# Optimization experiments

Measured on AMD Instinct MI355X. Metric: run time of the kernel, lower is better.

Reference implementation:

```python
import jax, jax.numpy as jnp
import numpy as np

B, I, H, L, D, O = 2048, 512, 512, 32, 1024, 512
TEMP = 1.0


def _make_params(key):
    ks = jax.random.split(key, 16)
    s = 0.05
    p = {}
    p['in_W'] = jax.random.normal(ks[0], (H, I), jnp.float32) * s
    p['in_b'] = jnp.zeros((H,), jnp.float32)
    p['out_W'] = jax.random.normal(ks[1], (O, H), jnp.float32) * s
    p['out_b'] = jnp.zeros((O,), jnp.float32)
    p['enc_Wih'] = jax.random.normal(ks[2], (4 * H, H), jnp.float32) * s
    p['enc_Whh'] = jax.random.normal(ks[3], (4 * H, H), jnp.float32) * s
    p['enc_bih'] = jnp.zeros((4 * H,), jnp.float32)
    p['enc_bhh'] = jnp.zeros((4 * H,), jnp.float32)
    p['dec_Wih'] = jax.random.normal(ks[4], (4 * H, H), jnp.float32) * s
    p['dec_Whh'] = jax.random.normal(ks[5], (4 * H, H), jnp.float32) * s
    p['dec_bih'] = jnp.zeros((4 * H,), jnp.float32)
    p['dec_bhh'] = jnp.zeros((4 * H,), jnp.float32)
    p['h2t_W'] = jax.random.normal(ks[6], (D, H), jnp.float32) * s
    p['h2t_b'] = jnp.zeros((D,), jnp.float32)
    p['t2h_W'] = jax.random.normal(ks[7], (H, D), jnp.float32) * s
    p['t2h_b'] = jnp.zeros((H,), jnp.float32)
    return p


def setup_inputs() -> dict:
    key = jax.random.key(0)
    k1, k2, k3 = jax.random.split(key, 3)
    inp = {'x': jax.random.normal(k1, (B, I), jnp.float32),
           'gumbel': jax.random.gumbel(k2, (L, B, D), jnp.float32)}
    inp.update(_make_params(k3))
    return inp


def _lstm_cell(x, h, c, Wih, Whh, bih, bhh):
    gates = x @ Wih.T + bih + h @ Whh.T + bhh  # [B, 4H]
    i, f, g, o = jnp.split(gates, 4, axis=-1)
    i = jax.nn.sigmoid(i); f = jax.nn.sigmoid(f)
    g = jnp.tanh(g); o = jax.nn.sigmoid(o)
    c_new = f * c + i * g
    h_new = o * jnp.tanh(c_new)
    return h_new, c_new


def reference(x, gumbel, in_W, in_b, out_W, out_b,
              enc_Wih, enc_Whh, enc_bih, enc_bhh,
              dec_Wih, dec_Whh, dec_bih, dec_bhh,
              h2t_W, h2t_b, t2h_W, t2h_b):
    # ---- encode ----
    x_emb = x @ in_W.T + in_b                      # [B, H]
    hx0 = jnp.zeros((B, H), x.dtype)
    inp0 = jnp.zeros((B, H), x.dtype)

    def enc_step(carry, g_noise):
        hx, cx, inp = carry
        hx, cx = _lstm_cell(inp, hx, cx, enc_Wih, enc_Whh, enc_bih, enc_bhh)
        pre = hx @ h2t_W.T + h2t_b                 # [B, D]
        soft = jax.nn.softmax((pre + g_noise) / TEMP, axis=-1)
        amax = jnp.argmax(soft, axis=-1)           # [B]
        oh = jax.nn.one_hot(amax, D, dtype=soft.dtype)
        z = soft + jax.lax.stop_gradient(oh - soft)  # straight-through
        inp = z @ t2h_W.T + t2h_b
        return (hx, cx, inp), (z, pre, amax)

    # initial cell state is the embedded input (cx = x), per the source
    _, (z_seq, logit_seq, msg_seq) = jax.lax.scan(
        enc_step, (hx0, x_emb, inp0), gumbel)
    one_hot = jnp.transpose(z_seq, (1, 0, 2))      # [B, L, D]
    logits = jnp.transpose(logit_seq, (1, 0, 2))   # [B, L, D]
    messages = msg_seq.T                           # [B, L]

    # ---- decode ----
    z_emb = z_seq @ t2h_W.T + t2h_b                # [L, B, H]

    def dec_step(carry, inp):
        hx, cx = carry
        hx, cx = _lstm_cell(inp, hx, cx, dec_Wih, dec_Whh, dec_bih, dec_bhh)
        return (hx, cx), None

    (hx_final, _), _ = jax.lax.scan(
        dec_step, (jnp.zeros((B, H), x.dtype), jnp.zeros((B, H), x.dtype)), z_emb)
    recon = hx_final @ out_W.T + out_b             # [B, O]
    return recon, one_hot, logits, messages
```

## Files before the change

kernel.cpp:

```cpp
#include <hip/hip_runtime.h>
#include <math.h>

#define B_  2048
#define I_  512
#define H_  512
#define L_  32
#define D_  1024
#define O_  512
#define H4_ 2048
#define KC  32

typedef _Float16 f16x8 __attribute__((ext_vector_type(8)));
typedef _Float16 f16x4 __attribute__((ext_vector_type(4)));
typedef float    f32x4 __attribute__((ext_vector_type(4)));

#define SPLIT_S  1024.0f
#define SPLIT_RS 0.0009765625f

__device__ __forceinline__ void gload16(const _Float16* g, _Float16* l) {
    __builtin_amdgcn_global_load_lds(
        (const __attribute__((address_space(1))) void*)g,
        (__attribute__((address_space(3))) void*)l, 16, 0, 0);
}

__device__ __forceinline__ f16x8 lds_frag(const _Float16* base, int row, int ko) {
    int off = row * 64 + ((((ko >> 3) ^ (row & 7))) << 3);
    return *(const f16x8*)(base + off);
}

__global__ __launch_bounds__(256) void gemm_atb(
    const float* __restrict__ A, const float* __restrict__ W,
    const float* __restrict__ bias, float* __restrict__ C, int ldc,
    float* __restrict__ C2, int ldc2,
    int M, int N, int K)
{
    __shared__ __align__(16) float As[KC][68];
    __shared__ __align__(16) float Ws[KC][68];
    const int tx = threadIdx.x & 15, ty = threadIdx.x >> 4;
    const int m0 = blockIdx.y * 64, n0 = blockIdx.x * 64;
    float acc[4][4] = {};

    for (int k0 = 0; k0 < K; k0 += KC) {
#pragma unroll
        for (int p = 0; p < 2; ++p) {
            int q = threadIdx.x + 256 * p;
            int r = q >> 3, c = q & 7;
            float4 va = *reinterpret_cast<const float4*>(
                &A[(long long)(m0 + r) * K + k0 + c * 4]);
            As[c * 4 + 0][r] = va.x; As[c * 4 + 1][r] = va.y;
            As[c * 4 + 2][r] = va.z; As[c * 4 + 3][r] = va.w;
            float4 vw = *reinterpret_cast<const float4*>(
                &W[(long long)(n0 + r) * K + k0 + c * 4]);
            Ws[c * 4 + 0][r] = vw.x; Ws[c * 4 + 1][r] = vw.y;
            Ws[c * 4 + 2][r] = vw.z; Ws[c * 4 + 3][r] = vw.w;
        }
        __syncthreads();
#pragma unroll
        for (int kk = 0; kk < KC; ++kk) {
            float4 a = *reinterpret_cast<const float4*>(&As[kk][ty * 4]);
            float4 w = *reinterpret_cast<const float4*>(&Ws[kk][tx * 4]);
            float av[4] = {a.x, a.y, a.z, a.w};
            float wv[4] = {w.x, w.y, w.z, w.w};
#pragma unroll
            for (int i = 0; i < 4; ++i)
#pragma unroll
                for (int j = 0; j < 4; ++j)
                    acc[i][j] = fmaf(av[i], wv[j], acc[i][j]);
        }
        __syncthreads();
    }

#pragma unroll
    for (int i = 0; i < 4; ++i) {
        int m = m0 + ty * 4 + i;
        int n = n0 + tx * 4;
        float4 out;
        out.x = acc[i][0]; out.y = acc[i][1]; out.z = acc[i][2]; out.w = acc[i][3];
        if (bias) {
            out.x += bias[n + 0]; out.y += bias[n + 1];
            out.z += bias[n + 2]; out.w += bias[n + 3];
        }
        *reinterpret_cast<float4*>(&C[(long long)m * ldc + n]) = out;
        if (C2)
            *reinterpret_cast<float4*>(&C2[(long long)m * ldc2 + n]) = out;
    }
}

__global__ __launch_bounds__(256) void split_f16(
    const float* __restrict__ src, _Float16* __restrict__ d1,
    _Float16* __restrict__ d2, int n4)
{
    int i = blockIdx.x * 256 + threadIdx.x;
    if (i >= n4) return;
    float4 v = reinterpret_cast<const float4*>(src)[i];
    float vv[4] = {v.x, v.y, v.z, v.w};
    f16x4 o1, o2;
#pragma unroll
    for (int j = 0; j < 4; ++j) {
        _Float16 hh = (_Float16)vv[j];
        o1[j] = hh;
        o2[j] = (_Float16)((vv[j] - (float)hh) * SPLIT_S);
    }
    *reinterpret_cast<f16x4*>(d1 + 4 * i) = o1;
    *reinterpret_cast<f16x4*>(d2 + 4 * i) = o2;
}

__global__ __launch_bounds__(256) void gemm_mfma_atb(
    const _Float16* __restrict__ A1, const _Float16* __restrict__ A2,
    const _Float16* __restrict__ W1, const _Float16* __restrict__ W2,
    float* __restrict__ C, int N, int K)
{
    __shared__ __align__(16) _Float16 As1[64 * 64];
    __shared__ __align__(16) _Float16 As2[64 * 64];
    __shared__ __align__(16) _Float16 Ws1[64 * 64];
    __shared__ __align__(16) _Float16 Ws2[64 * 64];

    const int tid = threadIdx.x;
    const int m0 = blockIdx.y * 64, n0 = blockIdx.x * 64;
    const int ln = tid & 63, wid = tid >> 6;
    const int wm = wid >> 1, wn = wid & 1;

    f32x4 accM[2][2] = {};
    f32x4 accC[2][2] = {};

    for (int k0 = 0; k0 < K; k0 += 64) {
        int jsw = ((ln & 7) ^ (ln >> 3)) << 3;
#pragma unroll
        for (int s = 0; s < 2; ++s) {
            int seg = wid + s * 4;
            int r   = seg * 8 + (ln >> 3);
            size_t ga = (size_t)(m0 + r) * K + k0 + jsw;
            gload16(A1 + ga, &As1[seg * 512]);
            gload16(A2 + ga, &As2[seg * 512]);
            size_t gw = (size_t)(n0 + r) * K + k0 + jsw;
            gload16(W1 + gw, &Ws1[seg * 512]);
            gload16(W2 + gw, &Ws2[seg * 512]);
        }
        __syncthreads();
        const int ac = (ln >> 4) << 3;
        const int arow = wm * 32 + (ln & 15);
        const int brow = wn * 32 + (ln & 15);
#pragma unroll
        for (int kc = 0; kc < 2; ++kc) {
            int ko = kc * 32 + ac;
            f16x8 b1[2], b2[2];
#pragma unroll
            for (int fn = 0; fn < 2; ++fn) {
                b1[fn] = lds_frag(Ws1, brow + fn * 16, ko);
                b2[fn] = lds_frag(Ws2, brow + fn * 16, ko);
            }
#pragma unroll
            for (int fm = 0; fm < 2; ++fm) {
                f16x8 a1 = lds_frag(As1, arow + fm * 16, ko);
                f16x8 a2 = lds_frag(As2, arow + fm * 16, ko);
#pragma unroll
                for (int fn = 0; fn < 2; ++fn) {
                    accM[fm][fn] = __builtin_amdgcn_mfma_f32_16x16x32_f16(
                        a1, b1[fn], accM[fm][fn], 0, 0, 0);
                    accC[fm][fn] = __builtin_amdgcn_mfma_f32_16x16x32_f16(
                        a1, b2[fn], accC[fm][fn], 0, 0, 0);
                    accC[fm][fn] = __builtin_amdgcn_mfma_f32_16x16x32_f16(
                        a2, b1[fn], accC[fm][fn], 0, 0, 0);
                }
            }
        }
        __syncthreads();
    }

    const int hl = ln & 15;
    const int rb = m0 + wm * 32 + ((ln >> 4) << 2);
#pragma unroll
    for (int fn = 0; fn < 2; ++fn) {
        int d = n0 + wn * 32 + fn * 16 + hl;
#pragma unroll
        for (int fm = 0; fm < 2; ++fm)
#pragma unroll
            for (int rg = 0; rg < 4; ++rg) {
                int b = rb + fm * 16 + rg;
                C[(size_t)b * N + d] =
                    accM[fm][fn][rg] + SPLIT_RS * accC[fm][fn][rg];
            }
    }
}

__global__ __launch_bounds__(256) void lstm_fused(
    const _Float16* __restrict__ ehx1, const _Float16* __restrict__ ehx2,
    float* __restrict__ ecx,
    const _Float16* __restrict__ eW1, const _Float16* __restrict__ eW2,
    const float* __restrict__ Pe,
    const float* __restrict__ ebih, const float* __restrict__ ebhh,
    _Float16* __restrict__ eho1, _Float16* __restrict__ eho2,
    const _Float16* __restrict__ dhx1, const _Float16* __restrict__ dhx2,
    float* __restrict__ dcx,
    const _Float16* __restrict__ dW1, const _Float16* __restrict__ dW2,
    const float* __restrict__ Pd,
    const float* __restrict__ dbih, const float* __restrict__ dbhh,
    _Float16* __restrict__ dho1, _Float16* __restrict__ dho2,
    float* __restrict__ hof,
    const float* __restrict__ pbest, const int* __restrict__ pidx,
    int have_gather,
    float* __restrict__ onehot, float* __restrict__ messages, int lmsg,
    int encdec)
{
    __shared__ __align__(16) _Float16 As1[64 * 64];
    __shared__ __align__(16) _Float16 As2[64 * 64];
    __shared__ __align__(16) _Float16 Ws1[128 * 64];
    __shared__ __align__(16) _Float16 Ws2[128 * 64];
    __shared__ int ms[64];

    const int tid = threadIdx.x;
    const int m0 = blockIdx.y * 64, h0 = blockIdx.x * 32;
    const int ln = tid & 63, wid = tid >> 6;
    const int wm = wid >> 1, wn = wid & 1;
    const int role = (encdec == 3) ? (int)blockIdx.z : ((encdec & 1) ? 0 : 1);

    const _Float16* hx1 = role ? dhx1 : ehx1;
    const _Float16* hx2 = role ? dhx2 : ehx2;
    float*          cx  = role ? dcx  : ecx;
    const _Float16* W1  = role ? dW1  : eW1;
    const _Float16* W2  = role ? dW2  : eW2;
    const float*    P   = role ? Pd   : Pe;
    const float*    bih = role ? dbih : ebih;
    const float*    bhh = role ? dbhh : ebhh;
    _Float16*       ho1 = role ? dho1 : eho1;
    _Float16*       ho2 = role ? dho2 : eho2;

    if (have_gather && tid < 64) {
        int b = m0 + tid;
        const float* pb = pbest + (size_t)b * 16;
        const int*   pi = pidx  + (size_t)b * 16;
        float best = -INFINITY; int bi = 0;
#pragma unroll
        for (int j = 0; j < 16; ++j) {
            float v = pb[j]; int i = pi[j];
            if (v > best || (v == best && i < bi)) { best = v; bi = i; }
        }
        ms[tid] = bi;
        if (lmsg >= 0 && blockIdx.z == 0 && blockIdx.x == 0) {
            messages[(size_t)b * L_ + lmsg] = (float)bi;
            onehot[((size_t)b * L_ + lmsg) * D_ + bi] = 1.0f;
        }
    }

    f32x4 accM[2][4] = {};
    f32x4 accC[2][4] = {};

    for (int k0 = 0; k0 < H_; k0 += 64) {
        int jsw = ((ln & 7) ^ (ln >> 3)) << 3;
#pragma unroll
        for (int s = 0; s < 2; ++s) {
            int seg = wid + s * 4;
            int r   = seg * 8 + (ln >> 3);
            size_t ga = (size_t)(m0 + r) * H_ + k0 + jsw;
            gload16(hx1 + ga, &As1[seg * 512]);
            gload16(hx2 + ga, &As2[seg * 512]);
        }
#pragma unroll
        for (int s = 0; s < 4; ++s) {
            int seg = wid + s * 4;
            int r   = seg * 8 + (ln >> 3);
            int wrow = ((r >> 4) & 3) * H_ + h0 + ((r >> 6) << 4) + (r & 15);
            size_t gw = (size_t)wrow * H_ + k0 + jsw;
            gload16(W1 + gw, &Ws1[seg * 512]);
            gload16(W2 + gw, &Ws2[seg * 512]);
        }
        __syncthreads();
        const int ac = (ln >> 4) << 3;
        const int arow = wm * 32 + (ln & 15);
        const int brow = wn * 64 + (ln & 15);
#pragma unroll
        for (int kc = 0; kc < 2; ++kc) {
            int ko = kc * 32 + ac;
            f16x8 b1[4], b2[4];
#pragma unroll
            for (int fn = 0; fn < 4; ++fn) {
                b1[fn] = lds_frag(Ws1, brow + fn * 16, ko);
                b2[fn] = lds_frag(Ws2, brow + fn * 16, ko);
            }
#pragma unroll
            for (int fm = 0; fm < 2; ++fm) {
                f16x8 a1 = lds_frag(As1, arow + fm * 16, ko);
                f16x8 a2 = lds_frag(As2, arow + fm * 16, ko);
#pragma unroll
                for (int fn = 0; fn < 4; ++fn) {
                    accM[fm][fn] = __builtin_amdgcn_mfma_f32_16x16x32_f16(
                        a1, b1[fn], accM[fm][fn], 0, 0, 0);
                    accC[fm][fn] = __builtin_amdgcn_mfma_f32_16x16x32_f16(
                        a1, b2[fn], accC[fm][fn], 0, 0, 0);
                    accC[fm][fn] = __builtin_amdgcn_mfma_f32_16x16x32_f16(
                        a2, b1[fn], accC[fm][fn], 0, 0, 0);
                }
            }
        }
        __syncthreads();
    }

    const int hl = ln & 15;
    const int h  = h0 + wn * 16 + hl;
    const int rb = m0 + wm * 32 + ((ln >> 4) << 2);
    float bs0 = bih[0 * H_ + h] + bhh[0 * H_ + h];
    float bs1 = bih[1 * H_ + h] + bhh[1 * H_ + h];
    float bs2 = bih[2 * H_ + h] + bhh[2 * H_ + h];
    float bs3 = bih[3 * H_ + h] + bhh[3 * H_ + h];
#pragma unroll
    for (int fm = 0; fm < 2; ++fm) {
#pragma unroll
        for (int rg = 0; rg < 4; ++rg) {
            int b = rb + fm * 16 + rg;
            float g0 = accM[fm][0][rg] + SPLIT_RS * accC[fm][0][rg] + bs0;
            float g1 = accM[fm][1][rg] + SPLIT_RS * accC[fm][1][rg] + bs1;
            float g2 = accM[fm][2][rg] + SPLIT_RS * accC[fm][2][rg] + bs2;
            float g3 = accM[fm][3][rg] + SPLIT_RS * accC[fm][3][rg] + bs3;
            if (have_gather) {
                const float* Pr = P + (size_t)ms[b - m0] * H4_;
                g0 += Pr[0 * H_ + h]; g1 += Pr[1 * H_ + h];
                g2 += Pr[2 * H_ + h]; g3 += Pr[3 * H_ + h];
            }
            float ig = 1.f / (1.f + expf(-g0));
            float fg = 1.f / (1.f + expf(-g1));
            float gg = tanhf(g2);
            float og = 1.f / (1.f + expf(-g3));
            size_t off = (size_t)b * H_ + h;
            float cnew = fg * cx[off] + ig * gg;
            cx[off] = cnew;
            float hv = og * tanhf(cnew);
            _Float16 hh1 = (_Float16)hv;
            ho1[off] = hh1;
            ho2[off] = (_Float16)((hv - (float)hh1) * SPLIT_S);
            if (role && hof != nullptr) hof[off] = hv;
        }
    }
}

__global__ __launch_bounds__(256) void gemm_pre_fused(
    const _Float16* __restrict__ A1, const _Float16* __restrict__ A2,
    const _Float16* __restrict__ W1, const _Float16* __restrict__ W2,
    const float* __restrict__ bias,
    float* __restrict__ C2, int ldc2,
    const float* __restrict__ gum,
    float* __restrict__ pbest, int* __restrict__ pidx)
{
    __shared__ __align__(16) _Float16 As1[64 * 64];
    __shared__ __align__(16) _Float16 As2[64 * 64];
    __shared__ __align__(16) _Float16 Ws1[64 * 64];
    __shared__ __align__(16) _Float16 Ws2[64 * 64];
    __shared__ float cb[2][64];
    __shared__ int   ci[2][64];

    const int tid = threadIdx.x;
    const int m0 = blockIdx.y * 64, n0 = blockIdx.x * 64;
    const int ln = tid & 63, wid = tid >> 6;
    const int wm = wid >> 1, wn = wid & 1;

    f32x4 accM[2][2] = {};
    f32x4 accC[2][2] = {};

    for (int k0 = 0; k0 < H_; k0 += 64) {
        int jsw = ((ln & 7) ^ (ln >> 3)) << 3;
#pragma unroll
        for (int s = 0; s < 2; ++s) {
            int seg = wid + s * 4;
            int r   = seg * 8 + (ln >> 3);
            size_t ga = (size_t)(m0 + r) * H_ + k0 + jsw;
            gload16(A1 + ga, &As1[seg * 512]);
            gload16(A2 + ga, &As2[seg * 512]);
        }
#pragma unroll
        for (int s = 0; s < 2; ++s) {
            int seg = wid + s * 4;
            int r   = seg * 8 + (ln >> 3);
            size_t gw = (size_t)(n0 + r) * H_ + k0 + jsw;
            gload16(W1 + gw, &Ws1[seg * 512]);
            gload16(W2 + gw, &Ws2[seg * 512]);
        }
        __syncthreads();
        const int ac = (ln >> 4) << 3;
        const int arow = wm * 32 + (ln & 15);
        const int brow = wn * 32 + (ln & 15);
#pragma unroll
        for (int kc = 0; kc < 2; ++kc) {
            int ko = kc * 32 + ac;
            f16x8 b1[2], b2[2];
#pragma unroll
            for (int fn = 0; fn < 2; ++fn) {
                b1[fn] = lds_frag(Ws1, brow + fn * 16, ko);
                b2[fn] = lds_frag(Ws2, brow + fn * 16, ko);
            }
#pragma unroll
            for (int fm = 0; fm < 2; ++fm) {
                f16x8 a1 = lds_frag(As1, arow + fm * 16, ko);
                f16x8 a2 = lds_frag(As2, arow + fm * 16, ko);
#pragma unroll
                for (int fn = 0; fn < 2; ++fn) {
                    accM[fm][fn] = __builtin_amdgcn_mfma_f32_16x16x32_f16(
                        a1, b1[fn], accM[fm][fn], 0, 0, 0);
                    accC[fm][fn] = __builtin_amdgcn_mfma_f32_16x16x32_f16(
                        a1, b2[fn], accC[fm][fn], 0, 0, 0);
                    accC[fm][fn] = __builtin_amdgcn_mfma_f32_16x16x32_f16(
                        a2, b1[fn], accC[fm][fn], 0, 0, 0);
                }
            }
        }
        __syncthreads();
    }

    const int hl = ln & 15;
    const int g4 = ln >> 4;
    const int rb = m0 + wm * 32 + (g4 << 2);
    float vbest[2][4]; int vidx[2][4];
#pragma unroll
    for (int fm = 0; fm < 2; ++fm)
#pragma unroll
        for (int rg = 0; rg < 4; ++rg) { vbest[fm][rg] = -INFINITY; vidx[fm][rg] = 0; }

#pragma unroll
    for (int fn = 0; fn < 2; ++fn) {
        int d = n0 + wn * 32 + fn * 16 + hl;
        float bv = bias[d];
#pragma unroll
        for (int fm = 0; fm < 2; ++fm)
#pragma unroll
            for (int rg = 0; rg < 4; ++rg) {
                int b = rb + fm * 16 + rg;
                float v = accM[fm][fn][rg] + SPLIT_RS * accC[fm][fn][rg] + bv;
                C2[(size_t)b * ldc2 + d] = v;
                float t = v + gum[(size_t)b * D_ + d];
                if (t > vbest[fm][rg]) { vbest[fm][rg] = t; vidx[fm][rg] = d; }
            }
    }

#pragma unroll
    for (int off = 1; off < 16; off <<= 1) {
#pragma unroll
        for (int fm = 0; fm < 2; ++fm)
#pragma unroll
            for (int rg = 0; rg < 4; ++rg) {
                float ov = __shfl_xor(vbest[fm][rg], off);
                int   oi = __shfl_xor(vidx[fm][rg], off);
                if (ov > vbest[fm][rg] ||
                    (ov == vbest[fm][rg] && oi < vidx[fm][rg])) {
                    vbest[fm][rg] = ov; vidx[fm][rg] = oi;
                }
            }
    }
    if (hl == 0) {
#pragma unroll
        for (int fm = 0; fm < 2; ++fm)
#pragma unroll
            for (int rg = 0; rg < 4; ++rg) {
                int rl = wm * 32 + fm * 16 + (g4 << 2) + rg;
                cb[wn][rl] = vbest[fm][rg];
                ci[wn][rl] = vidx[fm][rg];
            }
    }
    __syncthreads();
    if (tid < 64) {
        float b0 = cb[0][tid]; int i0 = ci[0][tid];
        float b1v = cb[1][tid]; int i1 = ci[1][tid];
        if (b1v > b0 || (b1v == b0 && i1 < i0)) { b0 = b1v; i0 = i1; }
        pbest[(size_t)(m0 + tid) * 16 + blockIdx.x] = b0;
        pidx [(size_t)(m0 + tid) * 16 + blockIdx.x] = i0;
    }
}

__global__ __launch_bounds__(256) void build_emb(
    const float* __restrict__ t2h_W, const float* __restrict__ t2h_b,
    float* __restrict__ emb)
{
    int idx = blockIdx.x * 256 + threadIdx.x;
    int d = idx >> 9, h = idx & (H_ - 1);
    emb[idx] = t2h_W[(long long)h * D_ + d] + t2h_b[h];
}

extern "C" void kernel_launch(void* const* d_in, const int* in_sizes, int n_in,
                              void* d_out, int out_size, void* d_ws, size_t ws_size,
                              hipStream_t stream)
{
    (void)in_sizes; (void)n_in; (void)out_size; (void)ws_size;
    const float* x       = (const float*)d_in[0];
    const float* gumbel  = (const float*)d_in[1];
    const float* in_W    = (const float*)d_in[2];
    const float* in_b    = (const float*)d_in[3];
    const float* out_W   = (const float*)d_in[4];
    const float* out_b   = (const float*)d_in[5];
    const float* enc_Wih = (const float*)d_in[6];
    const float* enc_Whh = (const float*)d_in[7];
    const float* enc_bih = (const float*)d_in[8];
    const float* enc_bhh = (const float*)d_in[9];
    const float* dec_Wih = (const float*)d_in[10];
    const float* dec_Whh = (const float*)d_in[11];
    const float* dec_bih = (const float*)d_in[12];
    const float* dec_bhh = (const float*)d_in[13];
    const float* h2t_W   = (const float*)d_in[14];
    const float* h2t_b   = (const float*)d_in[15];
    const float* t2h_W   = (const float*)d_in[16];
    const float* t2h_b   = (const float*)d_in[17];

    float* out      = (float*)d_out;
    float* recon    = out;
    float* onehot   = out + (size_t)B_ * O_;
    float* logits   = onehot + (size_t)B_ * L_ * D_;
    float* messages = logits + (size_t)B_ * L_ * D_;

    float* ws    = (float*)d_ws;
    float* ecx   = ws;
    float* dcx   = ecx + (size_t)B_ * H_;
    float* emb   = dcx + (size_t)B_ * H_;
    float* P_enc = emb + (size_t)D_ * H_;
    float* P_dec = P_enc + (size_t)D_ * H4_;
    float* hxf   = P_dec + (size_t)D_ * H4_;
    float* pbest = hxf + (size_t)B_ * H_;
    int*   pidx  = (int*)(pbest + (size_t)B_ * 16);
    _Float16* fb   = (_Float16*)(pidx + (size_t)B_ * 16);
    _Float16* ehA1 = fb;  fb += (size_t)B_ * H_;
    _Float16* ehA2 = fb;  fb += (size_t)B_ * H_;
    _Float16* ehB1 = fb;  fb += (size_t)B_ * H_;
    _Float16* ehB2 = fb;  fb += (size_t)B_ * H_;
    _Float16* dhA1 = fb;  fb += (size_t)B_ * H_;
    _Float16* dhA2 = fb;  fb += (size_t)B_ * H_;
    _Float16* dhB1 = fb;  fb += (size_t)B_ * H_;
    _Float16* dhB2 = fb;  fb += (size_t)B_ * H_;
    _Float16* encW1 = fb; fb += (size_t)H4_ * H_;
    _Float16* encW2 = fb; fb += (size_t)H4_ * H_;
    _Float16* decW1 = fb; fb += (size_t)H4_ * H_;
    _Float16* decW2 = fb; fb += (size_t)H4_ * H_;
    _Float16* h2t1  = fb; fb += (size_t)D_ * H_;
    _Float16* h2t2  = fb; fb += (size_t)D_ * H_;
    _Float16* embs1 = fb; fb += (size_t)D_ * H_;
    _Float16* embs2 = fb; fb += (size_t)D_ * H_;
    _Float16* eWih1 = fb; fb += (size_t)H4_ * H_;
    _Float16* eWih2 = fb; fb += (size_t)H4_ * H_;
    _Float16* dWih1 = fb; fb += (size_t)H4_ * H_;
    _Float16* dWih2 = fb;

    const dim3 blk256(256);

    (void)hipMemsetAsync(ehA1, 0, (size_t)B_ * H_ * 4, stream);
    (void)hipMemsetAsync(dhA1, 0, (size_t)B_ * H_ * 4, stream);
    (void)hipMemsetAsync(dcx, 0, (size_t)B_ * H_ * sizeof(float), stream);
    (void)hipMemsetAsync(onehot, 0, (size_t)B_ * L_ * D_ * sizeof(float), stream);

    split_f16<<<dim3((H4_ * H_ / 4) / 256), blk256, 0, stream>>>(
        enc_Whh, encW1, encW2, H4_ * H_ / 4);
    split_f16<<<dim3((H4_ * H_ / 4) / 256), blk256, 0, stream>>>(
        dec_Whh, decW1, decW2, H4_ * H_ / 4);
    split_f16<<<dim3((D_ * H_ / 4) / 256), blk256, 0, stream>>>(
        h2t_W, h2t1, h2t2, D_ * H_ / 4);
    split_f16<<<dim3((H4_ * H_ / 4) / 256), blk256, 0, stream>>>(
        enc_Wih, eWih1, eWih2, H4_ * H_ / 4);
    split_f16<<<dim3((H4_ * H_ / 4) / 256), blk256, 0, stream>>>(
        dec_Wih, dWih1, dWih2, H4_ * H_ / 4);

    gemm_atb<<<dim3(H_ / 64, B_ / 64), blk256, 0, stream>>>(
        x, in_W, in_b, ecx, H_, nullptr, 0, B_, H_, I_);

    build_emb<<<dim3((D_ * H_) / 256), blk256, 0, stream>>>(t2h_W, t2h_b, emb);
    split_f16<<<dim3((D_ * H_ / 4) / 256), blk256, 0, stream>>>(
        emb, embs1, embs2, D_ * H_ / 4);
    gemm_mfma_atb<<<dim3(H4_ / 64, D_ / 64), blk256, 0, stream>>>(
        embs1, embs2, eWih1, eWih2, P_enc, H4_, H_);
    gemm_mfma_atb<<<dim3(H4_ / 64, D_ / 64), blk256, 0, stream>>>(
        embs1, embs2, dWih1, dWih2, P_dec, H4_, H_);

    _Float16* e1[2] = {ehA1, ehB1};
    _Float16* e2[2] = {ehA2, ehB2};
    _Float16* d1[2] = {dhA1, dhB1};
    _Float16* d2[2] = {dhA2, dhB2};

    for (int l = 0; l < L_; ++l) {
        int ein = l & 1, eo = ein ^ 1;
        int din = (l - 1) & 1, do_ = din ^ 1;
        lstm_fused<<<dim3(H_ / 32, B_ / 64, l ? 2 : 1), blk256, 0, stream>>>(
            e1[ein], e2[ein], ecx, encW1, encW2, P_enc, enc_bih, enc_bhh,
            e1[eo], e2[eo],
            l ? d1[din] : nullptr, l ? d2[din] : nullptr, dcx,
            decW1, decW2, P_dec, dec_bih, dec_bhh,
            l ? d1[do_] : nullptr, l ? d2[do_] : nullptr,
            nullptr, pbest, pidx, l ? 1 : 0,
            onehot, messages, l - 1, l ? 3 : 1);
        gemm_pre_fused<<<dim3(D_ / 64, B_ / 64), blk256, 0, stream>>>(
            e1[eo], e2[eo], h2t1, h2t2, h2t_b,
            logits + (size_t)l * D_, L_ * D_,
            gumbel + (size_t)l * B_ * D_, pbest, pidx);
    }

    lstm_fused<<<dim3(H_ / 32, B_ / 64, 1), blk256, 0, stream>>>(
        nullptr, nullptr, ecx, encW1, encW2, P_enc, enc_bih, enc_bhh,
        nullptr, nullptr,
        d1[1], d2[1], dcx, decW1, decW2, P_dec, dec_bih, dec_bhh,
        d1[0], d2[0],
        hxf, pbest, pidx, 1,
        onehot, messages, L_ - 1, 2);

    gemm_atb<<<dim3(O_ / 64, B_ / 64), blk256, 0, stream>>>(
        hxf, out_W, out_b, recon, O_, nullptr, 0, B_, O_, H_);
}
```

Before: 2.848 ms.

## Move input/output projections to split-fp16 MFMA and enlarge LSTM row tile

Replaces the scalar fp32 GEMM used for the input embedding and the final output projection with the split-fp16 MFMA GEMM, adding a bias epilogue and split kernels for x, in_W and out_W. The output projection now reads the fp16 hi/lo hidden state directly, so the fp32 final-hidden buffer is dropped. Separately, the fused LSTM kernel now tiles 128 batch rows per block instead of 64, doubling accumulators and LDS use. The aim is more reuse of the recurrent weight tile across rows, at the cost of half as many blocks and higher register and LDS pressure.

```diff
diff --git a/kernel.cpp b/kernel.cpp
--- a/kernel.cpp
+++ b/kernel.cpp
@@ -8,7 +8,6 @@
 #define D_  1024
 #define O_  512
 #define H4_ 2048
-#define KC  32
 
 typedef _Float16 f16x8 __attribute__((ext_vector_type(8)));
 typedef _Float16 f16x4 __attribute__((ext_vector_type(4)));
@@ -26,64 +25,6 @@
 __device__ __forceinline__ f16x8 lds_frag(const _Float16* base, int row, int ko) {
     int off = row * 64 + ((((ko >> 3) ^ (row & 7))) << 3);
     return *(const f16x8*)(base + off);
-}
-
-__global__ __launch_bounds__(256) void gemm_atb(
-    const float* __restrict__ A, const float* __restrict__ W,
-    const float* __restrict__ bias, float* __restrict__ C, int ldc,
-    float* __restrict__ C2, int ldc2,
-    int M, int N, int K)
-{
-    __shared__ __align__(16) float As[KC][68];
-    __shared__ __align__(16) float Ws[KC][68];
-    const int tx = threadIdx.x & 15, ty = threadIdx.x >> 4;
-    const int m0 = blockIdx.y * 64, n0 = blockIdx.x * 64;
-    float acc[4][4] = {};
-
-    for (int k0 = 0; k0 < K; k0 += KC) {
-#pragma unroll
-        for (int p = 0; p < 2; ++p) {
-            int q = threadIdx.x + 256 * p;
-            int r = q >> 3, c = q & 7;
-            float4 va = *reinterpret_cast<const float4*>(
-                &A[(long long)(m0 + r) * K + k0 + c * 4]);
-            As[c * 4 + 0][r] = va.x; As[c * 4 + 1][r] = va.y;
-            As[c * 4 + 2][r] = va.z; As[c * 4 + 3][r] = va.w;
-            float4 vw = *reinterpret_cast<const float4*>(
-                &W[(long long)(n0 + r) * K + k0 + c * 4]);
-            Ws[c * 4 + 0][r] = vw.x; Ws[c * 4 + 1][r] = vw.y;
-            Ws[c * 4 + 2][r] = vw.z; Ws[c * 4 + 3][r] = vw.w;
-        }
-        __syncthreads();
-#pragma unroll
-        for (int kk = 0; kk < KC; ++kk) {
-            float4 a = *reinterpret_cast<const float4*>(&As[kk][ty * 4]);
-            float4 w = *reinterpret_cast<const float4*>(&Ws[kk][tx * 4]);
-            float av[4] = {a.x, a.y, a.z, a.w};
-            float wv[4] = {w.x, w.y, w.z, w.w};
-#pragma unroll
-            for (int i = 0; i < 4; ++i)
-#pragma unroll
-                for (int j = 0; j < 4; ++j)
-                    acc[i][j] = fmaf(av[i], wv[j], acc[i][j]);
-        }
-        __syncthreads();
-    }
-
-#pragma unroll
-    for (int i = 0; i < 4; ++i) {
-        int m = m0 + ty * 4 + i;
-        int n = n0 + tx * 4;
-        float4 out;
-        out.x = acc[i][0]; out.y = acc[i][1]; out.z = acc[i][2]; out.w = acc[i][3];
-        if (bias) {
-            out.x += bias[n + 0]; out.y += bias[n + 1];
-            out.z += bias[n + 2]; out.w += bias[n + 3];
-        }
-        *reinterpret_cast<float4*>(&C[(long long)m * ldc + n]) = out;
-        if (C2)
-            *reinterpret_cast<float4*>(&C2[(long long)m * ldc2 + n]) = out;
-    }
 }
 
 __global__ __launch_bounds__(256) void split_f16(
@@ -108,6 +49,7 @@
 __global__ __launch_bounds__(256) void gemm_mfma_atb(
     const _Float16* __restrict__ A1, const _Float16* __restrict__ A2,
     const _Float16* __restrict__ W1, const _Float16* __restrict__ W2,
+    const float* __restrict__ bias,
     float* __restrict__ C, int N, int K)
 {
     __shared__ __align__(16) _Float16 As1[64 * 64];
@@ -172,13 +114,14 @@
 #pragma unroll
     for (int fn = 0; fn < 2; ++fn) {
         int d = n0 + wn * 32 + fn * 16 + hl;
+        float bv = bias ? bias[d] : 0.f;
 #pragma unroll
         for (int fm = 0; fm < 2; ++fm)
 #pragma unroll
             for (int rg = 0; rg < 4; ++rg) {
                 int b = rb + fm * 16 + rg;
                 C[(size_t)b * N + d] =
-                    accM[fm][fn][rg] + SPLIT_RS * accC[fm][fn][rg];
+                    accM[fm][fn][rg] + SPLIT_RS * accC[fm][fn][rg] + bv;
             }
     }
 }
@@ -196,20 +139,19 @@
     const float* __restrict__ Pd,
     const float* __restrict__ dbih, const float* __restrict__ dbhh,
     _Float16* __restrict__ dho1, _Float16* __restrict__ dho2,
-    float* __restrict__ hof,
     const float* __restrict__ pbest, const int* __restrict__ pidx,
     int have_gather,
     float* __restrict__ onehot, float* __restrict__ messages, int lmsg,
     int encdec)
 {
-    __shared__ __align__(16) _Float16 As1[64 * 64];
-    __shared__ __align__(16) _Float16 As2[64 * 64];
+    __shared__ __align__(16) _Float16 As1[128 * 64];
+    __shared__ __align__(16) _Float16 As2[128 * 64];
     __shared__ __align__(16) _Float16 Ws1[128 * 64];
     __shared__ __align__(16) _Float16 Ws2[128 * 64];
-    __shared__ int ms[64];
+    __shared__ int ms[128];
 
     const int tid = threadIdx.x;
-    const int m0 = blockIdx.y * 64, h0 = blockIdx.x * 32;
+    const int m0 = blockIdx.y * 128, h0 = blockIdx.x * 32;
     const int ln = tid & 63, wid = tid >> 6;
     const int wm = wid >> 1, wn = wid & 1;
     const int role = (encdec == 3) ? (int)blockIdx.z : ((encdec & 1) ? 0 : 1);
@@ -225,7 +167,7 @@
     _Float16*       ho1 = role ? dho1 : eho1;
     _Float16*       ho2 = role ? dho2 : eho2;
 
-    if (have_gather && tid < 64) {
+    if (have_gather && tid < 128) {
         int b = m0 + tid;
         const float* pb = pbest + (size_t)b * 16;
         const int*   pi = pidx  + (size_t)b * 16;
@@ -242,13 +184,13 @@
         }
     }
 
-    f32x4 accM[2][4] = {};
-    f32x4 accC[2][4] = {};
+    f32x4 accM[4][4] = {};
+    f32x4 accC[4][4] = {};
 
     for (int k0 = 0; k0 < H_; k0 += 64) {
         int jsw = ((ln & 7) ^ (ln >> 3)) << 3;
 #pragma unroll
-        for (int s = 0; s < 2; ++s) {
+        for (int s = 0; s < 4; ++s) {
             int seg = wid + s * 4;
             int r   = seg * 8 + (ln >> 3);
             size_t ga = (size_t)(m0 + r) * H_ + k0 + jsw;
@@ -266,7 +208,7 @@
         }
         __syncthreads();
         const int ac = (ln >> 4) << 3;
-        const int arow = wm * 32 + (ln & 15);
+        const int arow = wm * 64 + (ln & 15);
         const int brow = wn * 64 + (ln & 15);
 #pragma unroll
         for (int kc = 0; kc < 2; ++kc) {
@@ -278,7 +220,7 @@
                 b2[fn] = lds_frag(Ws2, brow + fn * 16, ko);
             }
 #pragma unroll
-            for (int fm = 0; fm < 2; ++fm) {
+            for (int fm = 0; fm < 4; ++fm) {
                 f16x8 a1 = lds_frag(As1, arow + fm * 16, ko);
                 f16x8 a2 = lds_frag(As2, arow + fm * 16, ko);
 #pragma unroll
@@ -297,13 +239,13 @@
 
     const int hl = ln & 15;
     const int h  = h0 + wn * 16 + hl;
-    const int rb = m0 + wm * 32 + ((ln >> 4) << 2);
+    const int rb = m0 + wm * 64 + ((ln >> 4) << 2);
     float bs0 = bih[0 * H_ + h] + bhh[0 * H_ + h];
     float bs1 = bih[1 * H_ + h] + bhh[1 * H_ + h];
     float bs2 = bih[2 * H_ + h] + bhh[2 * H_ + h];
     float bs3 = bih[3 * H_ + h] + bhh[3 * H_ + h];
 #pragma unroll
-    for (int fm = 0; fm < 2; ++fm) {
+    for (int fm = 0; fm < 4; ++fm) {
 #pragma unroll
         for (int rg = 0; rg < 4; ++rg) {
             int b = rb + fm * 16 + rg;
@@ -327,7 +269,6 @@
             _Float16 hh1 = (_Float16)hv;
             ho1[off] = hh1;
             ho2[off] = (_Float16)((hv - (float)hh1) * SPLIT_S);
-            if (role && hof != nullptr) hof[off] = hv;
         }
     }
 }
@@ -508,8 +449,7 @@
     float* emb   = dcx + (size_t)B_ * H_;
     float* P_enc = emb + (size_t)D_ * H_;
     float* P_dec = P_enc + (size_t)D_ * H4_;
-    float* hxf   = P_dec + (size_t)D_ * H4_;
-    float* pbest = hxf + (size_t)B_ * H_;
+    float* pbest = P_dec + (size_t)D_ * H4_;
     int*   pidx  = (int*)(pbest + (size_t)B_ * 16);
     _Float16* fb   = (_Float16*)(pidx + (size_t)B_ * 16);
     _Float16* ehA1 = fb;  fb += (size_t)B_ * H_;
@@ -531,7 +471,13 @@
     _Float16* eWih1 = fb; fb += (size_t)H4_ * H_;
     _Float16* eWih2 = fb; fb += (size_t)H4_ * H_;
     _Float16* dWih1 = fb; fb += (size_t)H4_ * H_;
-    _Float16* dWih2 = fb;
+    _Float16* dWih2 = fb; fb += (size_t)H4_ * H_;
+    _Float16* xs1   = fb; fb += (size_t)B_ * I_;
+    _Float16* xs2   = fb; fb += (size_t)B_ * I_;
+    _Float16* inW1  = fb; fb += (size_t)H_ * I_;
+    _Float16* inW2  = fb; fb += (size_t)H_ * I_;
+    _Float16* outW1 = fb; fb += (size_t)O_ * H_;
+    _Float16* outW2 = fb;
 
     const dim3 blk256(256);
 
@@ -550,17 +496,23 @@
         enc_Wih, eWih1, eWih2, H4_ * H_ / 4);
     split_f16<<<dim3((H4_ * H_ / 4) / 256), blk256, 0, stream>>>(
         dec_Wih, dWih1, dWih2, H4_ * H_ / 4);
-
-    gemm_atb<<<dim3(H_ / 64, B_ / 64), blk256, 0, stream>>>(
-        x, in_W, in_b, ecx, H_, nullptr, 0, B_, H_, I_);
+    split_f16<<<dim3((B_ * I_ / 4) / 256), blk256, 0, stream>>>(
+        x, xs1, xs2, B_ * I_ / 4);
+    split_f16<<<dim3((H_ * I_ / 4) / 256), blk256, 0, stream>>>(
+        in_W, inW1, inW2, H_ * I_ / 4);
+    split_f16<<<dim3((O_ * H_ / 4) / 256), blk256, 0, stream>>>(
+        out_W, outW1, outW2, O_ * H_ / 4);
+
+    gemm_mfma_atb<<<dim3(H_ / 64, B_ / 64), blk256, 0, stream>>>(
+        xs1, xs2, inW1, inW2, in_b, ecx, H_, I_);
 
     build_emb<<<dim3((D_ * H_) / 256), blk256, 0, stream>>>(t2h_W, t2h_b, emb);
     split_f16<<<dim3((D_ * H_ / 4) / 256), blk256, 0, stream>>>(
         emb, embs1, embs2, D_ * H_ / 4);
     gemm_mfma_atb<<<dim3(H4_ / 64, D_ / 64), blk256, 0, stream>>>(
-        embs1, embs2, eWih1, eWih2, P_enc, H4_, H_);
+        embs1, embs2, eWih1, eWih2, nullptr, P_enc, H4_, H_);
     gemm_mfma_atb<<<dim3(H4_ / 64, D_ / 64), blk256, 0, stream>>>(
-        embs1, embs2, dWih1, dWih2, P_dec, H4_, H_);
+        embs1, embs2, dWih1, dWih2, nullptr, P_dec, H4_, H_);
 
     _Float16* e1[2] = {ehA1, ehB1};
     _Float16* e2[2] = {ehA2, ehB2};
@@ -570,13 +522,13 @@
     for (int l = 0; l < L_; ++l) {
         int ein = l & 1, eo = ein ^ 1;
         int din = (l - 1) & 1, do_ = din ^ 1;
-        lstm_fused<<<dim3(H_ / 32, B_ / 64, l ? 2 : 1), blk256, 0, stream>>>(
+        lstm_fused<<<dim3(H_ / 32, B_ / 128, l ? 2 : 1), blk256, 0, stream>>>(
             e1[ein], e2[ein], ecx, encW1, encW2, P_enc, enc_bih, enc_bhh,
             e1[eo], e2[eo],
             l ? d1[din] : nullptr, l ? d2[din] : nullptr, dcx,
             decW1, decW2, P_dec, dec_bih, dec_bhh,
             l ? d1[do_] : nullptr, l ? d2[do_] : nullptr,
-            nullptr, pbest, pidx, l ? 1 : 0,
+            pbest, pidx, l ? 1 : 0,
             onehot, messages, l - 1, l ? 3 : 1);
         gemm_pre_fused<<<dim3(D_ / 64, B_ / 64), blk256, 0, stream>>>(
             e1[eo], e2[eo], h2t1, h2t2, h2t_b,
@@ -584,14 +536,14 @@
             gumbel + (size_t)l * B_ * D_, pbest, pidx);
     }
 
-    lstm_fused<<<dim3(H_ / 32, B_ / 64, 1), blk256, 0, stream>>>(
+    lstm_fused<<<dim3(H_ / 32, B_ / 128, 1), blk256, 0, stream>>>(
         nullptr, nullptr, ecx, encW1, encW2, P_enc, enc_bih, enc_bhh,
         nullptr, nullptr,
         d1[1], d2[1], dcx, decW1, decW2, P_dec, dec_bih, dec_bhh,
         d1[0], d2[0],
-        hxf, pbest, pidx, 1,
+        pbest, pidx, 1,
         onehot, messages, L_ - 1, 2);
 
-    gemm_atb<<<dim3(O_ / 64, B_ / 64), blk256, 0, stream>>>(
-        hxf, out_W, out_b, recon, O_, nullptr, 0, B_, O_, H_);
-}
+    gemm_mfma_atb<<<dim3(O_ / 64, B_ / 64), blk256, 0, stream>>>(
+        d1[0], d2[0], outW1, outW2, out_b, recon, O_, H_);
+}
```

Result: slower. 3.409 ms (+19.7%).
